# Kernel optimization log

Measured on AMD Instinct MI355X. Metric: run time of the kernel, lower is better.

The kernel has to match this reference:

```python
import jax, jax.numpy as jnp
import numpy as np

MULT = 4
HIDDEN = 4096
HC_DIM = MULT * HIDDEN              # 16384
MIX_HC = (2 + MULT) * MULT          # 24 = n (pre) + n (post) + n*n (res)
NORM_EPS = 1e-6
SINK_EPS = 1e-6
POST_MULT = 1.0
SINK_ITERS = 10
B = 4096


def setup_inputs() -> dict:
    key = jax.random.key(0)
    k = jax.random.split(key, 7)
    return {
        "x_prev": jax.random.normal(k[0], (B, HIDDEN), jnp.float32),
        "residual_prev": jax.random.normal(k[1], (B, MULT, HIDDEN), jnp.float32),
        "post_mix_prev": jax.random.uniform(k[2], (B, MULT), jnp.float32),
        "comb_mix_prev": jax.random.uniform(k[3], (B, MULT, MULT), jnp.float32),
        # fn scaled so logits stay O(1) after the hc_dim-wide contraction
        "fn": jax.random.normal(k[4], (MIX_HC, HC_DIM), jnp.float32) * 0.01,
        "base": jax.random.normal(k[5], (MIX_HC,), jnp.float32) * 0.02,
        "scale": jax.random.uniform(k[6], (3,), jnp.float32),
    }


def _post_mapping(x, residual, post_mix, comb_mix):
    # residual_new[b,i,:] = sum_j comb[b,i,j] * residual[b,j,:] + post_mix[b,i] * x[b,:]
    return jnp.einsum('bij,bjh->bih', comb_mix, residual) + post_mix[:, :, None] * x[:, None, :]


def _pre_mapping(residual, fn, base, scale):
    n = MULT
    b = residual.shape[0]
    x_flat = residual.reshape(b, HC_DIM)
    # RMS norm over the full hyper-connection dim
    rms = jnp.sqrt(jnp.mean(x_flat * x_flat, axis=-1, keepdims=True) + NORM_EPS)
    x_norm = x_flat / rms
    logits = jnp.einsum('bd,md->bm', x_norm, fn)  # [B, mix_hc]
    pre = logits[:, :n] * scale[0] + base[:n]
    post = logits[:, n:2 * n] * scale[1] + base[n:2 * n]
    res = logits[:, 2 * n:] * scale[2] + base[2 * n:]
    # H_pre on simplex -> weights combining n streams into layer input
    h_pre = jax.nn.softmax(pre, axis=-1)                       # [B, n]
    post_mix = POST_MULT * jax.nn.sigmoid(post)[:, :, None]    # [B, n, 1]
    # H_res doubly stochastic via Sinkhorn-Knopp row/col normalization
    m = jnp.exp(res.reshape(b, n, n))
    def body(m, _):
        m = m / (m.sum(axis=-1, keepdims=True) + SINK_EPS)  # row normalize
        m = m / (m.sum(axis=-2, keepdims=True) + SINK_EPS)  # col normalize
        return m, None
    comb_mix, _ = jax.lax.scan(body, m, None, length=SINK_ITERS)
    layer_input = jnp.einsum('bn,bnh->bh', h_pre, residual)
    return post_mix, comb_mix, layer_input


def reference(x_prev, residual_prev, post_mix_prev, comb_mix_prev, fn, base, scale):
    residual_cur = _post_mapping(x_prev, residual_prev, post_mix_prev, comb_mix_prev)
    post_mix_cur, comb_mix_cur, layer_input_cur = _pre_mapping(residual_cur, fn, base, scale)
    return residual_cur, post_mix_cur, comb_mix_cur, layer_input_cur
```

## Files before the change

kernel.cpp:

```cpp
#include <hip/hip_runtime.h>
#include <math.h>

#define HIDDEN 4096
#define MULT 4
#define HCD 16384
#define MIX 24
#define BB 4096

#define KA_THREADS 512
#define ROWS 32
#define HSPLIT 8
#define HSLICE 512
#define TILE_H 64
#define NTILES 8
#define TILE_D 256

#define BAR() asm volatile("s_waitcnt lgkmcnt(0)\n\ts_barrier" ::: "memory")

__global__ __launch_bounds__(256) void k_transpose_fn(const float* __restrict__ fn,
                                                      float* __restrict__ fnT) {
    const int d = blockIdx.x * 256 + threadIdx.x;
    float v[MIX];
#pragma unroll
    for (int m = 0; m < MIX; ++m) v[m] = fn[(size_t)m * HCD + d];
    float4* dst = (float4*)(fnT + (size_t)d * MIX);
#pragma unroll
    for (int m4 = 0; m4 < MIX / 4; ++m4)
        dst[m4] = make_float4(v[4*m4+0], v[4*m4+1], v[4*m4+2], v[4*m4+3]);
}

__global__ __launch_bounds__(KA_THREADS, 4)
void k_main(const float* __restrict__ x_prev, const float* __restrict__ res_prev,
            const float* __restrict__ pm_prev, const float* __restrict__ comb_prev,
            const float* __restrict__ fnT, float* __restrict__ res_cur,
            float* __restrict__ part_lg, float* __restrict__ part_sq)
{
    __shared__ float A[ROWS * TILE_D];
    const int tid  = threadIdx.x;
    const int rg   = blockIdx.x >> 3;
    const int hq   = blockIdx.x & 7;
    const int row1 = tid >> 4;
    const int q    = tid & 15;
    const int b1   = rg * ROWS + row1;
    const int wid  = tid >> 6;
    const int lane = tid & 63;
    const int row2 = lane & 31;
    const int mh   = lane >> 5;

    float comb[MULT][MULT], pm[MULT];
#pragma unroll
    for (int i = 0; i < MULT; ++i) {
        pm[i] = pm_prev[(size_t)b1 * MULT + i];
#pragma unroll
        for (int j = 0; j < MULT; ++j)
            comb[i][j] = comb_prev[(size_t)b1 * 16 + i * 4 + j];
    }

    float acc[MIX];
#pragma unroll
    for (int m = 0; m < MIX; ++m) acc[m] = 0.f;
    float ssq = 0.f;

    const int sw1   = (row1 & 7) << 2;
    const int sw2   = (row2 & 7) << 2;
    const int i_str = wid >> 1;
    const int hoffb = (wid & 1) * 32;

#pragma unroll 1
    for (int t = 0; t < NTILES; ++t) {
        const int h0 = hq * HSLICE + t * TILE_H;
        const size_t gh = (size_t)h0 + q * 4;
        const float4 xv = *(const float4*)(x_prev + (size_t)b1 * HIDDEN + gh);
        float4 rv[MULT];
#pragma unroll
        for (int j = 0; j < MULT; ++j)
            rv[j] = *(const float4*)(res_prev + ((size_t)b1 * MULT + j) * HIDDEN + gh);
#pragma unroll
        for (int i = 0; i < MULT; ++i) {
            float4 r;
            r.x = pm[i] * xv.x; r.y = pm[i] * xv.y;
            r.z = pm[i] * xv.z; r.w = pm[i] * xv.w;
#pragma unroll
            for (int j = 0; j < MULT; ++j) {
                r.x += comb[i][j] * rv[j].x; r.y += comb[i][j] * rv[j].y;
                r.z += comb[i][j] * rv[j].z; r.w += comb[i][j] * rv[j].w;
            }
            *(float4*)(res_cur + ((size_t)b1 * MULT + i) * HIDDEN + gh) = r;
            ssq += r.x*r.x + r.y*r.y + r.z*r.z + r.w*r.w;
            const int dl = i * TILE_H + q * 4;
            *(float4*)(&A[row1 * TILE_D + (dl ^ sw1)]) = r;
        }
        BAR();
#pragma unroll
        for (int k = 0; k < 8; ++k) {
            const int dl = wid * 32 + k * 4;
            const float4 av = *(const float4*)(&A[row2 * TILE_D + (dl ^ sw2)]);
            const int dg = i_str * HIDDEN + h0 + hoffb + k * 4;
            const float* fp = fnT + (size_t)__builtin_amdgcn_readfirstlane(dg) * MIX;
#pragma unroll
            for (int m = 0; m < MIX; ++m) acc[m] += av.x * fp[m];
#pragma unroll
            for (int m = 0; m < MIX; ++m) acc[m] += av.y * fp[MIX + m];
#pragma unroll
            for (int m = 0; m < MIX; ++m) acc[m] += av.z * fp[2 * MIX + m];
#pragma unroll
            for (int m = 0; m < MIX; ++m) acc[m] += av.w * fp[3 * MIX + m];
        }
        BAR();
    }

    ssq += __shfl_down(ssq, 8);
    ssq += __shfl_down(ssq, 4);
    ssq += __shfl_down(ssq, 2);
    ssq += __shfl_down(ssq, 1);
    if (q == 0) part_sq[(size_t)hq * BB + b1] = ssq;

    {
        const int base = (row2 * 8 + wid) * 24 + mh * 12;
        if (mh == 0) {
#pragma unroll
            for (int j4 = 0; j4 < 3; ++j4)
                *(float4*)(&A[base + j4 * 4]) =
                    make_float4(acc[j4*4+0], acc[j4*4+1], acc[j4*4+2], acc[j4*4+3]);
        } else {
#pragma unroll
            for (int j4 = 0; j4 < 3; ++j4)
                *(float4*)(&A[base + j4 * 4]) =
                    make_float4(acc[12+j4*4+0], acc[12+j4*4+1], acc[12+j4*4+2], acc[12+j4*4+3]);
        }
    }
    BAR();
#pragma unroll 1
    for (int it = tid; it < ROWS * MIX; it += KA_THREADS) {
        const int row = it / MIX;
        const int m   = it - row * MIX;
        float s = 0.f;
#pragma unroll
        for (int w = 0; w < 8; ++w) s += A[(row * 8 + w) * 24 + m];
        part_lg[((size_t)hq * BB + rg * ROWS + row) * MIX + m] = s;
    }
}

__global__ __launch_bounds__(256) void k_post(
        const float* __restrict__ part_lg, const float* __restrict__ part_sq,
        const float* __restrict__ basep, const float* __restrict__ scale,
        const float* __restrict__ res_cur,
        float* __restrict__ post_mix, float* __restrict__ comb_out,
        float* __restrict__ layer_in)
{
    const int b   = blockIdx.x;
    const int tid = threadIdx.x;
    __shared__ float red[MIX + 1];
    __shared__ float hp_s[4];

    if (tid < MIX) {
        float s = 0.f;
#pragma unroll
        for (int w = 0; w < HSPLIT; ++w)
            s += part_lg[((size_t)w * BB + b) * MIX + tid];
        red[tid] = s;
    } else if (tid == MIX) {
        float s = 0.f;
#pragma unroll
        for (int w = 0; w < HSPLIT; ++w) s += part_sq[(size_t)w * BB + b];
        red[MIX] = s;
    }
    __syncthreads();

    if (tid == 0) {
        const float rms = sqrtf(red[MIX] * (1.0f / (float)HCD) + 1e-6f);
        const float inv = 1.0f / rms;
        const float s0 = scale[0], s1 = scale[1], s2 = scale[2];

        float pre[4], post[4], rr[16];
#pragma unroll
        for (int i = 0; i < 4; ++i)  pre[i]  = red[i]     * inv * s0 + basep[i];
#pragma unroll
        for (int i = 0; i < 4; ++i)  post[i] = red[4 + i] * inv * s1 + basep[4 + i];
#pragma unroll
        for (int k = 0; k < 16; ++k) rr[k]   = red[8 + k] * inv * s2 + basep[8 + k];

        const float mx = fmaxf(fmaxf(pre[0], pre[1]), fmaxf(pre[2], pre[3]));
        float e[4], es = 0.f;
#pragma unroll
        for (int i = 0; i < 4; ++i) { e[i] = expf(pre[i] - mx); es += e[i]; }
        const float esr = 1.0f / es;
#pragma unroll
        for (int i = 0; i < 4; ++i) hp_s[i] = e[i] * esr;

        float4 pmv = make_float4(1.f/(1.f+expf(-post[0])), 1.f/(1.f+expf(-post[1])),
                                 1.f/(1.f+expf(-post[2])), 1.f/(1.f+expf(-post[3])));
        *(float4*)(post_mix + (size_t)b * 4) = pmv;

        float M[16];
#pragma unroll
        for (int k = 0; k < 16; ++k) M[k] = expf(rr[k]);
#pragma unroll 1
        for (int it = 0; it < 10; ++it) {
#pragma unroll
            for (int i = 0; i < 4; ++i) {
                const float rs = 1.0f /
                    (M[i*4+0] + M[i*4+1] + M[i*4+2] + M[i*4+3] + 1e-6f);
#pragma unroll
                for (int j = 0; j < 4; ++j) M[i*4+j] *= rs;
            }
#pragma unroll
            for (int j = 0; j < 4; ++j) {
                const float cs = 1.0f /
                    (M[j] + M[4+j] + M[8+j] + M[12+j] + 1e-6f);
#pragma unroll
                for (int i = 0; i < 4; ++i) M[i*4+j] *= cs;
            }
        }
#pragma unroll
        for (int m4 = 0; m4 < 4; ++m4)
            *(float4*)(comb_out + (size_t)b * 16 + m4 * 4) =
                make_float4(M[4*m4+0], M[4*m4+1], M[4*m4+2], M[4*m4+3]);
    }
    __syncthreads();

    const float h0 = hp_s[0], h1 = hp_s[1], h2 = hp_s[2], h3 = hp_s[3];
    const float* rp = res_cur + (size_t)b * (MULT * HIDDEN);
    float* op = layer_in + (size_t)b * HIDDEN;
#pragma unroll
    for (int c = 0; c < 4; ++c) {
        const int c4 = (tid + c * 256) * 4;
        const float4 v0 = *(const float4*)(rp + 0 * HIDDEN + c4);
        const float4 v1 = *(const float4*)(rp + 1 * HIDDEN + c4);
        const float4 v2 = *(const float4*)(rp + 2 * HIDDEN + c4);
        const float4 v3 = *(const float4*)(rp + 3 * HIDDEN + c4);
        float4 o;
        o.x = h0*v0.x + h1*v1.x + h2*v2.x + h3*v3.x;
        o.y = h0*v0.y + h1*v1.y + h2*v2.y + h3*v3.y;
        o.z = h0*v0.z + h1*v1.z + h2*v2.z + h3*v3.z;
        o.w = h0*v0.w + h1*v1.w + h2*v2.w + h3*v3.w;
        *(float4*)(op + c4) = o;
    }
}

extern "C" void kernel_launch(void* const* d_in, const int* in_sizes, int n_in,
                              void* d_out, int out_size, void* d_ws, size_t ws_size,
                              hipStream_t stream) {
    const float* x_prev    = (const float*)d_in[0];
    const float* res_prev  = (const float*)d_in[1];
    const float* pm_prev   = (const float*)d_in[2];
    const float* comb_prev = (const float*)d_in[3];
    const float* fn        = (const float*)d_in[4];
    const float* base      = (const float*)d_in[5];
    const float* scale     = (const float*)d_in[6];

    float* out = (float*)d_out;
    float* res_cur  = out;
    float* post_mix = out + 67108864;
    float* comb_out = out + 67108864 + 16384;
    float* layer_in = out + 67108864 + 16384 + 65536;

    float* ws = (float*)d_ws;
    float* fnT     = ws;
    float* part_lg = ws + 393216;
    float* part_sq = ws + 393216 + 786432;

    k_transpose_fn<<<HCD / 256, 256, 0, stream>>>(fn, fnT);
    k_main<<<(BB / ROWS) * HSPLIT, KA_THREADS, 0, stream>>>(
        x_prev, res_prev, pm_prev, comb_prev, fnT, res_cur, part_lg, part_sq);
    k_post<<<BB, 256, 0, stream>>>(part_lg, part_sq, base, scale, res_cur,
                                   post_mix, comb_out, layer_in);
}
```

Baseline: 675.7 us.

## Split fused residual/logit kernel into separate residual and logit kernels

Replaces the fused kernel that computed the new residual and the fn projection via shared-memory tiles with two kernels. The first writes the residual and a per-row sum of squares. The second re-reads the residual with one row per lane and accumulates the 24 logits over 16 slices of the hc dim. This removes shared-memory staging and barriers. The cost is an extra full read of the residual from memory, plus a row-per-lane access pattern that strides lanes by a full row and so is poorly coalesced.

After: 1.056 ms. 1.56x slower.

```diff
diff --git a/kernel.cpp b/kernel.cpp
--- a/kernel.cpp
+++ b/kernel.cpp
@@ -7,15 +7,8 @@
 #define MIX 24
 #define BB 4096
 
-#define KA_THREADS 512
-#define ROWS 32
-#define HSPLIT 8
-#define HSLICE 512
-#define TILE_H 64
-#define NTILES 8
-#define TILE_D 256
-
-#define BAR() asm volatile("s_waitcnt lgkmcnt(0)\n\ts_barrier" ::: "memory")
+#define NSLICE 16
+#define DSLICE 1024
 
 __global__ __launch_bounds__(256) void k_transpose_fn(const float* __restrict__ fn,
                                                       float* __restrict__ fnT) {
@@ -29,52 +22,37 @@
         dst[m4] = make_float4(v[4*m4+0], v[4*m4+1], v[4*m4+2], v[4*m4+3]);
 }
 
-__global__ __launch_bounds__(KA_THREADS, 4)
-void k_main(const float* __restrict__ x_prev, const float* __restrict__ res_prev,
-            const float* __restrict__ pm_prev, const float* __restrict__ comb_prev,
-            const float* __restrict__ fnT, float* __restrict__ res_cur,
-            float* __restrict__ part_lg, float* __restrict__ part_sq)
+__global__ __launch_bounds__(256) void k_res(
+        const float* __restrict__ x_prev, const float* __restrict__ res_prev,
+        const float* __restrict__ pm_prev, const float* __restrict__ comb_prev,
+        float* __restrict__ res_cur, float* __restrict__ part_sq)
 {
-    __shared__ float A[ROWS * TILE_D];
-    const int tid  = threadIdx.x;
-    const int rg   = blockIdx.x >> 3;
-    const int hq   = blockIdx.x & 7;
-    const int row1 = tid >> 4;
-    const int q    = tid & 15;
-    const int b1   = rg * ROWS + row1;
-    const int wid  = tid >> 6;
-    const int lane = tid & 63;
-    const int row2 = lane & 31;
-    const int mh   = lane >> 5;
+    const int b   = blockIdx.x;
+    const int tid = threadIdx.x;
+    const int wid = tid >> 6, lane = tid & 63;
 
     float comb[MULT][MULT], pm[MULT];
 #pragma unroll
     for (int i = 0; i < MULT; ++i) {
-        pm[i] = pm_prev[(size_t)b1 * MULT + i];
+        pm[i] = pm_prev[(size_t)b * MULT + i];
 #pragma unroll
         for (int j = 0; j < MULT; ++j)
-            comb[i][j] = comb_prev[(size_t)b1 * 16 + i * 4 + j];
-    }
-
-    float acc[MIX];
-#pragma unroll
-    for (int m = 0; m < MIX; ++m) acc[m] = 0.f;
+            comb[i][j] = comb_prev[(size_t)b * 16 + i * 4 + j];
+    }
+
     float ssq = 0.f;
-
-    const int sw1   = (row1 & 7) << 2;
-    const int sw2   = (row2 & 7) << 2;
-    const int i_str = wid >> 1;
-    const int hoffb = (wid & 1) * 32;
-
-#pragma unroll 1
-    for (int t = 0; t < NTILES; ++t) {
-        const int h0 = hq * HSLICE + t * TILE_H;
-        const size_t gh = (size_t)h0 + q * 4;
-        const float4 xv = *(const float4*)(x_prev + (size_t)b1 * HIDDEN + gh);
+    const float* xb = x_prev   + (size_t)b * HIDDEN;
+    const float* rb = res_prev + (size_t)b * MULT * HIDDEN;
+    float*       ob = res_cur  + (size_t)b * MULT * HIDDEN;
+
+#pragma unroll
+    for (int c = 0; c < 4; ++c) {
+        const int h = (c * 256 + tid) * 4;
+        const float4 xv = *(const float4*)(xb + h);
         float4 rv[MULT];
 #pragma unroll
         for (int j = 0; j < MULT; ++j)
-            rv[j] = *(const float4*)(res_prev + ((size_t)b1 * MULT + j) * HIDDEN + gh);
+            rv[j] = *(const float4*)(rb + (size_t)j * HIDDEN + h);
 #pragma unroll
         for (int i = 0; i < MULT; ++i) {
             float4 r;
@@ -85,60 +63,55 @@
                 r.x += comb[i][j] * rv[j].x; r.y += comb[i][j] * rv[j].y;
                 r.z += comb[i][j] * rv[j].z; r.w += comb[i][j] * rv[j].w;
             }
-            *(float4*)(res_cur + ((size_t)b1 * MULT + i) * HIDDEN + gh) = r;
+            *(float4*)(ob + (size_t)i * HIDDEN + h) = r;
             ssq += r.x*r.x + r.y*r.y + r.z*r.z + r.w*r.w;
-            const int dl = i * TILE_H + q * 4;
-            *(float4*)(&A[row1 * TILE_D + (dl ^ sw1)]) = r;
         }
-        BAR();
-#pragma unroll
-        for (int k = 0; k < 8; ++k) {
-            const int dl = wid * 32 + k * 4;
-            const float4 av = *(const float4*)(&A[row2 * TILE_D + (dl ^ sw2)]);
-            const int dg = i_str * HIDDEN + h0 + hoffb + k * 4;
-            const float* fp = fnT + (size_t)__builtin_amdgcn_readfirstlane(dg) * MIX;
-#pragma unroll
-            for (int m = 0; m < MIX; ++m) acc[m] += av.x * fp[m];
-#pragma unroll
-            for (int m = 0; m < MIX; ++m) acc[m] += av.y * fp[MIX + m];
-#pragma unroll
-            for (int m = 0; m < MIX; ++m) acc[m] += av.z * fp[2 * MIX + m];
-#pragma unroll
-            for (int m = 0; m < MIX; ++m) acc[m] += av.w * fp[3 * MIX + m];
-        }
-        BAR();
-    }
-
-    ssq += __shfl_down(ssq, 8);
-    ssq += __shfl_down(ssq, 4);
-    ssq += __shfl_down(ssq, 2);
-    ssq += __shfl_down(ssq, 1);
-    if (q == 0) part_sq[(size_t)hq * BB + b1] = ssq;
-
-    {
-        const int base = (row2 * 8 + wid) * 24 + mh * 12;
-        if (mh == 0) {
-#pragma unroll
-            for (int j4 = 0; j4 < 3; ++j4)
-                *(float4*)(&A[base + j4 * 4]) =
-                    make_float4(acc[j4*4+0], acc[j4*4+1], acc[j4*4+2], acc[j4*4+3]);
-        } else {
-#pragma unroll
-            for (int j4 = 0; j4 < 3; ++j4)
-                *(float4*)(&A[base + j4 * 4]) =
-                    make_float4(acc[12+j4*4+0], acc[12+j4*4+1], acc[12+j4*4+2], acc[12+j4*4+3]);
-        }
-    }
-    BAR();
-#pragma unroll 1
-    for (int it = tid; it < ROWS * MIX; it += KA_THREADS) {
-        const int row = it / MIX;
-        const int m   = it - row * MIX;
-        float s = 0.f;
-#pragma unroll
-        for (int w = 0; w < 8; ++w) s += A[(row * 8 + w) * 24 + m];
-        part_lg[((size_t)hq * BB + rg * ROWS + row) * MIX + m] = s;
-    }
+    }
+
+#pragma unroll
+    for (int off = 32; off; off >>= 1) ssq += __shfl_down(ssq, off);
+    __shared__ float sred[4];
+    if (lane == 0) sred[wid] = ssq;
+    __syncthreads();
+    if (tid == 0) part_sq[b] = sred[0] + sred[1] + sred[2] + sred[3];
+}
+
+__global__ __launch_bounds__(256) void k_logit(
+        const float* __restrict__ res_cur, const float* __restrict__ fnT,
+        float* __restrict__ part_lg)
+{
+    const int wid  = threadIdx.x >> 6, lane = threadIdx.x & 63;
+    const int g    = blockIdx.x * 4 + wid;
+    const int rg   = g >> 4;
+    const int sl   = g & 15;
+    const int b    = rg * 64 + lane;
+
+    const float* rp  = res_cur + (size_t)b * HCD + (size_t)sl * DSLICE;
+    const float* fp0 = fnT + (size_t)sl * DSLICE * MIX;
+
+    float acc[MIX];
+#pragma unroll
+    for (int m = 0; m < MIX; ++m) acc[m] = 0.f;
+
+#pragma unroll 4
+    for (int ds = 0; ds < DSLICE / 4; ++ds) {
+        const float4 v  = *(const float4*)(rp + ds * 4);
+        const float* fp = fp0 + (size_t)ds * 4 * MIX;
+#pragma unroll
+        for (int m = 0; m < MIX; ++m) acc[m] += v.x * fp[m];
+#pragma unroll
+        for (int m = 0; m < MIX; ++m) acc[m] += v.y * fp[MIX + m];
+#pragma unroll
+        for (int m = 0; m < MIX; ++m) acc[m] += v.z * fp[2 * MIX + m];
+#pragma unroll
+        for (int m = 0; m < MIX; ++m) acc[m] += v.w * fp[3 * MIX + m];
+    }
+
+    float* dst = part_lg + ((size_t)sl * BB + b) * MIX;
+#pragma unroll
+    for (int m4 = 0; m4 < 6; ++m4)
+        *(float4*)(dst + m4 * 4) =
+            make_float4(acc[4*m4+0], acc[4*m4+1], acc[4*m4+2], acc[4*m4+3]);
 }
 
 __global__ __launch_bounds__(256) void k_post(
@@ -156,14 +129,11 @@
     if (tid < MIX) {
         float s = 0.f;
 #pragma unroll
-        for (int w = 0; w < HSPLIT; ++w)
+        for (int w = 0; w < NSLICE; ++w)
             s += part_lg[((size_t)w * BB + b) * MIX + tid];
         red[tid] = s;
     } else if (tid == MIX) {
-        float s = 0.f;
-#pragma unroll
-        for (int w = 0; w < HSPLIT; ++w) s += part_sq[(size_t)w * BB + b];
-        red[MIX] = s;
+        red[MIX] = part_sq[b];
     }
     __syncthreads();
 
@@ -258,11 +228,12 @@
     float* ws = (float*)d_ws;
     float* fnT     = ws;
     float* part_lg = ws + 393216;
-    float* part_sq = ws + 393216 + 786432;
+    float* part_sq = ws + 393216 + 1572864;
 
     k_transpose_fn<<<HCD / 256, 256, 0, stream>>>(fn, fnT);
-    k_main<<<(BB / ROWS) * HSPLIT, KA_THREADS, 0, stream>>>(
-        x_prev, res_prev, pm_prev, comb_prev, fnT, res_cur, part_lg, part_sq);
+    k_res<<<BB, 256, 0, stream>>>(x_prev, res_prev, pm_prev, comb_prev,
+                                  res_cur, part_sq);
+    k_logit<<<256, 256, 0, stream>>>(res_cur, fnT, part_lg);
     k_post<<<BB, 256, 0, stream>>>(part_lg, part_sq, base, scale, res_cur,
                                    post_mix, comb_out, layer_in);
 }
```
